# Performance work log

Hardware: AMD Instinct MI355X
Metric: run time of the kernel (lower is better)

## Reference

```python
import jax, jax.numpy as jnp
import numpy as np
import math

B, LQ, LK = 16, 64, 256
EMBED_TIME = 128
H = 8
DK = EMBED_TIME // H  # 16
DIM = 48              # input_dim (num clinical variables)
NHIDDEN = 128


def setup_inputs() -> dict:
    key = jax.random.key(0)
    ks = jax.random.split(key, 10)
    query = jax.random.normal(ks[0], (B, LQ, EMBED_TIME), dtype=jnp.float32)
    key_t = jax.random.normal(ks[1], (B, LK, EMBED_TIME), dtype=jnp.float32)
    value = jax.random.normal(ks[2], (B, LK, DIM), dtype=jnp.float32)
    mask = jax.random.randint(ks[3], (B, LK, DIM), 0, 2, dtype=jnp.int32)
    s = 0.02
    Wq = jax.random.normal(ks[4], (EMBED_TIME, EMBED_TIME), dtype=jnp.float32) * s
    bq = jnp.zeros((EMBED_TIME,), dtype=jnp.float32)
    Wk = jax.random.normal(ks[5], (EMBED_TIME, EMBED_TIME), dtype=jnp.float32) * s
    bk = jnp.zeros((EMBED_TIME,), dtype=jnp.float32)
    Wo = jax.random.normal(ks[6], (NHIDDEN, DIM * H), dtype=jnp.float32) * s
    bo = jnp.zeros((NHIDDEN,), dtype=jnp.float32)
    return {"query": query, "key": key_t, "value": value, "mask": mask,
            "Wq": Wq, "bq": bq, "Wk": Wk, "bk": bk, "Wo": Wo, "bo": bo}


def reference(query, key, value, mask, Wq, bq, Wk, bk, Wo, bo):
    # query: [B, Lq, E], key: [B, Lk, E], value: [B, Lk, D], mask: [B, Lk, D]
    b, lk, d = value.shape
    # time-embedding projections, split into heads: [B, H, L, DK]
    q = (query @ Wq.T + bq).reshape(b, -1, H, DK).transpose(0, 2, 1, 3)
    k = (key @ Wk.T + bk).reshape(b, -1, H, DK).transpose(0, 2, 1, 3)
    # scores: [B, H, Lq, Lk]
    scores = jnp.einsum('bhqd,bhkd->bhqk', q, k) / math.sqrt(DK)
    # expand over value dim (original repeat_interleave) -> [B, H, Lq, Lk, D]
    scores = scores[..., None]
    mask5 = mask[:, None, None, :, :]  # [B,1,1,Lk,D]
    scores = jnp.where(mask5 == 0, jnp.float32(-10000.0), scores)
    # softmax over the key/time axis (-2), per value-dimension
    p_attn = jax.nn.softmax(scores, axis=-2)  # [B,H,Lq,Lk,D]
    # weighted sum over keys: value broadcast over heads & queries
    x = jnp.sum(p_attn * value[:, None, None, :, :], axis=-2)  # [B,H,Lq,D]
    x = x.transpose(0, 2, 1, 3).reshape(b, -1, H * d)  # [B,Lq,H*D]
    return x @ Wo.T + bo  # [B, Lq, nhidden]
```

## Files before the change

### kernel.cpp

```cpp
#include <hip/hip_runtime.h>

#define BB 16
#define LQ 64
#define LK 256
#define EM 128
#define NH 8
#define DKK 16
#define DIM 48
#define NHID 128

#define QP_OFF  0
#define KP_OFF  (BB*LQ*EM)
#define XX_OFF  (KP_OFF + BB*LK*EM)
#define MVM_OFF (XX_OFF + BB*LQ*NH*DIM)

__global__ __launch_bounds__(128) void proj_prep_kernel(
    const float* __restrict__ query, const float* __restrict__ key,
    const float* __restrict__ value, const int* __restrict__ mask,
    const float* __restrict__ Wq, const float* __restrict__ bq,
    const float* __restrict__ Wk, const float* __restrict__ bk,
    float* __restrict__ ws)
{
    int bid = blockIdx.x;
    int t = threadIdx.x;
    if (bid < 640) {
        __shared__ __align__(16) float sX[8][EM];
        int row0 = bid * 8;
        const float* X; const float* W; const float* bias; float* out; int base;
        if (row0 < BB * LQ) { X = query; W = Wq; bias = bq; out = ws + QP_OFF; base = row0; }
        else                { X = key;   W = Wk; bias = bk; out = ws + KP_OFF; base = row0 - BB * LQ; }

        {
            const float4* src = (const float4*)(X + (size_t)base * EM);
            float4* dst = (float4*)(&sX[0][0]);
            #pragma unroll
            for (int u = 0; u < 2; u++) dst[t + u * 128] = src[t + u * 128];
        }
        __syncthreads();

        float acc[8];
        #pragma unroll
        for (int r = 0; r < 8; r++) acc[r] = 0.f;

        const float4* w4 = (const float4*)(W + (size_t)t * EM);
        #pragma unroll 8
        for (int k4 = 0; k4 < EM / 4; k4++) {
            float4 w = w4[k4];
            #pragma unroll
            for (int r = 0; r < 8; r++) {
                float4 x = ((const float4*)sX[r])[k4];
                acc[r] += x.x * w.x + x.y * w.y + x.z * w.z + x.w * w.w;
            }
        }
        float bb = bias[t];
        #pragma unroll
        for (int r = 0; r < 8; r++) out[(size_t)(base + r) * EM + t] = acc[r] + bb;
    } else {
        int p = bid - 640;
        int b = p >> 3, ks = p & 7;
        const float* vb = value + ((size_t)b * LK + ks * 32) * DIM;
        const int*   mb = mask  + ((size_t)b * LK + ks * 32) * DIM;
        float* ob = ws + MVM_OFF + ((size_t)b * LK + ks * 32) * 96;
        #pragma unroll
        for (int u = 0; u < 6; ++u) {
            int f = t + 128 * u;
            int r = f / 24, c = f - r * 24;
            float4 o;
            if (c < 12) {
                float4 v = *(const float4*)(vb + r * DIM + c * 4);
                int4  m  = *(const int4*)  (mb + r * DIM + c * 4);
                o.x = m.x ? v.x : 0.f; o.y = m.y ? v.y : 0.f;
                o.z = m.z ? v.z : 0.f; o.w = m.w ? v.w : 0.f;
            } else {
                int4 m = *(const int4*)(mb + r * DIM + (c - 12) * 4);
                o.x = m.x ? 1.f : 0.f; o.y = m.y ? 1.f : 0.f;
                o.z = m.z ? 1.f : 0.f; o.w = m.w ? 1.f : 0.f;
            }
            *(float4*)(ob + r * 96 + c * 4) = o;
        }
    }
}

__global__ __launch_bounds__(256) void attn_kernel(
    const float* __restrict__ qp, const float* __restrict__ kp,
    const float* __restrict__ mvm, float* __restrict__ xx)
{
    __shared__ __align__(16) float sQ[16][DKK];
    __shared__ __align__(16) float sE[LK][20];
    __shared__ __align__(16) float sW[64][100];

    int bid = blockIdx.x;
    int b  = bid >> 5;
    int h  = (bid >> 2) & 7;
    int q0 = (bid & 3) * 16;
    int t  = threadIdx.x;

    const float4* krp = (const float4*)(kp + ((size_t)b * LK + t) * EM + h * DKK);
    float4 k0 = krp[0], k1 = krp[1], k2 = krp[2], k3 = krp[3];
    if (t < 64) {
        int row = t >> 2, u = t & 3;
        *(float4*)&sQ[row][u * 4] =
            *(const float4*)(qp + ((size_t)b * LQ + q0 + row) * EM + h * DKK + u * 4);
    }
    __syncthreads();

    #pragma unroll
    for (int q4 = 0; q4 < 4; ++q4) {
        float4 ev;
        float* evp = (float*)&ev;
        #pragma unroll
        for (int qi = 0; qi < 4; ++qi) {
            const float4* qr = (const float4*)sQ[q4 * 4 + qi];
            float4 a = qr[0], c = qr[1], d = qr[2], e2 = qr[3];
            float s = k0.x*a.x + k0.y*a.y + k0.z*a.z + k0.w*a.w
                    + k1.x*c.x + k1.y*c.y + k1.z*c.z + k1.w*c.w
                    + k2.x*d.x + k2.y*d.y + k2.z*d.z + k2.w*d.w
                    + k3.x*e2.x + k3.y*e2.y + k3.z*e2.z + k3.w*e2.w;
            evp[qi] = __expf(s * 0.25f);
        }
        *(float4*)&sE[t][q4 * 4] = ev;
    }

    const float* mvb = mvm + (size_t)b * LK * 96;
    auto stage = [&](int kq) {
        const float* src = mvb + (size_t)kq * 64 * 96;
        #pragma unroll
        for (int u = 0; u < 6; ++u) {
            int f = t + 256 * u;
            int r = f / 24, c = f - r * 24;
            *(float4*)&sW[r][c * 4] = *(const float4*)(src + r * 96 + c * 4);
        }
    };
    stage(0);
    __syncthreads();

    int q  = t & 15;
    int kl = (t >> 4) & 3;
    int w  = t >> 6;

    float4 acc[6];
    #pragma unroll
    for (int c = 0; c < 6; ++c) acc[c] = make_float4(0.f, 0.f, 0.f, 0.f);

    for (int kq = 0; kq < 4; ++kq) {
        #pragma unroll 4
        for (int i = 0; i < 16; ++i) {
            int k = kl + 4 * i;
            float ev = sE[kq * 64 + k][q];
            const float4* row = (const float4*)&sW[k][0];
            #pragma unroll
            for (int c = 0; c < 6; ++c) {
                float4 m = row[w * 6 + c];
                acc[c].x += ev * m.x; acc[c].y += ev * m.y;
                acc[c].z += ev * m.z; acc[c].w += ev * m.w;
            }
        }
        __syncthreads();
        if (kq < 3) { stage(kq + 1); __syncthreads(); }
    }

    #pragma unroll
    for (int c = 0; c < 6; ++c) {
        acc[c].x += __shfl_xor(acc[c].x, 16, 64);
        acc[c].y += __shfl_xor(acc[c].y, 16, 64);
        acc[c].z += __shfl_xor(acc[c].z, 16, 64);
        acc[c].w += __shfl_xor(acc[c].w, 16, 64);
        acc[c].x += __shfl_xor(acc[c].x, 32, 64);
        acc[c].y += __shfl_xor(acc[c].y, 32, 64);
        acc[c].z += __shfl_xor(acc[c].z, 32, 64);
        acc[c].w += __shfl_xor(acc[c].w, 32, 64);
    }

    float* zbuf = &sW[0][0];
    if (kl == 0 && w >= 2) {
        #pragma unroll
        for (int c = 0; c < 6; ++c)
            *(float4*)&zbuf[q * 48 + (w - 2) * 24 + c * 4] = acc[c];
    }
    __syncthreads();
    if (kl == 0 && w < 2) {
        float* xr = xx + ((size_t)b * LQ + q0 + q) * (NH * DIM) + h * DIM + w * 24;
        #pragma unroll
        for (int c = 0; c < 6; ++c) {
            float4 z = *(const float4*)&zbuf[q * 48 + w * 24 + c * 4];
            float4 n = acc[c];
            float4 r;
            r.x = n.x / z.x; r.y = n.y / z.y; r.z = n.z / z.z; r.w = n.w / z.w;
            *(float4*)(xr + c * 4) = r;
        }
    }
}

__global__ __launch_bounds__(128) void outproj_kernel(
    const float* __restrict__ x, const float* __restrict__ Wo,
    const float* __restrict__ bo, float* __restrict__ out)
{
    __shared__ __align__(16) float sX[4][NH * DIM];
    int row0 = blockIdx.x * 4;
    int t = threadIdx.x;
    {
        const float4* src = (const float4*)(x + (size_t)row0 * (NH * DIM));
        float4* dst = (float4*)(&sX[0][0]);
        #pragma unroll
        for (int u = 0; u < 3; u++) dst[t + u * 128] = src[t + u * 128];
    }
    __syncthreads();

    float acc[4] = {0.f, 0.f, 0.f, 0.f};
    const float4* w4 = (const float4*)(Wo + (size_t)t * (NH * DIM));
    #pragma unroll 8
    for (int k4 = 0; k4 < (NH * DIM) / 4; k4++) {
        float4 w = w4[k4];
        #pragma unroll
        for (int r = 0; r < 4; r++) {
            float4 xv = ((const float4*)sX[r])[k4];
            acc[r] += xv.x * w.x + xv.y * w.y + xv.z * w.z + xv.w * w.w;
        }
    }
    float bb = bo[t];
    #pragma unroll
    for (int r = 0; r < 4; r++) out[(size_t)(row0 + r) * NHID + t] = acc[r] + bb;
}

extern "C" void kernel_launch(void* const* d_in, const int* in_sizes, int n_in,
                              void* d_out, int out_size, void* d_ws, size_t ws_size,
                              hipStream_t stream) {
    const float* query = (const float*)d_in[0];
    const float* key   = (const float*)d_in[1];
    const float* value = (const float*)d_in[2];
    const int*   mask  = (const int*)  d_in[3];
    const float* Wq    = (const float*)d_in[4];
    const float* bq    = (const float*)d_in[5];
    const float* Wk    = (const float*)d_in[6];
    const float* bk    = (const float*)d_in[7];
    const float* Wo    = (const float*)d_in[8];
    const float* bo    = (const float*)d_in[9];
    float* out = (float*)d_out;
    float* ws = (float*)d_ws;

    proj_prep_kernel<<<dim3(768), dim3(128), 0, stream>>>(
        query, key, value, mask, Wq, bq, Wk, bk, ws);
    attn_kernel<<<dim3(BB * NH * 4), dim3(256), 0, stream>>>(
        ws + QP_OFF, ws + KP_OFF, ws + MVM_OFF, ws + XX_OFF);
    outproj_kernel<<<dim3(BB * LQ / 4), dim3(128), 0, stream>>>(
        ws + XX_OFF, Wo, bo, out);
}
```

Baseline: 53.01 us.

## Fuse mask/value prep into attention kernel and register-tile the accumulation

```diff
diff --git a/kernel.cpp b/kernel.cpp
--- a/kernel.cpp
+++ b/kernel.cpp
@@ -9,84 +9,57 @@
 #define DIM 48
 #define NHID 128
 
-#define QP_OFF  0
-#define KP_OFF  (BB*LQ*EM)
-#define XX_OFF  (KP_OFF + BB*LK*EM)
-#define MVM_OFF (XX_OFF + BB*LQ*NH*DIM)
-
-__global__ __launch_bounds__(128) void proj_prep_kernel(
+#define QP_OFF 0
+#define KP_OFF (BB*LQ*EM)
+#define XX_OFF (KP_OFF + BB*LK*EM)
+
+__global__ __launch_bounds__(128) void proj_kernel(
     const float* __restrict__ query, const float* __restrict__ key,
-    const float* __restrict__ value, const int* __restrict__ mask,
     const float* __restrict__ Wq, const float* __restrict__ bq,
     const float* __restrict__ Wk, const float* __restrict__ bk,
     float* __restrict__ ws)
 {
-    int bid = blockIdx.x;
+    __shared__ __align__(16) float sX[8][EM];
+    int row0 = blockIdx.x * 8;
     int t = threadIdx.x;
-    if (bid < 640) {
-        __shared__ __align__(16) float sX[8][EM];
-        int row0 = bid * 8;
-        const float* X; const float* W; const float* bias; float* out; int base;
-        if (row0 < BB * LQ) { X = query; W = Wq; bias = bq; out = ws + QP_OFF; base = row0; }
-        else                { X = key;   W = Wk; bias = bk; out = ws + KP_OFF; base = row0 - BB * LQ; }
-
-        {
-            const float4* src = (const float4*)(X + (size_t)base * EM);
-            float4* dst = (float4*)(&sX[0][0]);
-            #pragma unroll
-            for (int u = 0; u < 2; u++) dst[t + u * 128] = src[t + u * 128];
-        }
-        __syncthreads();
-
-        float acc[8];
-        #pragma unroll
-        for (int r = 0; r < 8; r++) acc[r] = 0.f;
-
-        const float4* w4 = (const float4*)(W + (size_t)t * EM);
-        #pragma unroll 8
-        for (int k4 = 0; k4 < EM / 4; k4++) {
-            float4 w = w4[k4];
-            #pragma unroll
-            for (int r = 0; r < 8; r++) {
-                float4 x = ((const float4*)sX[r])[k4];
-                acc[r] += x.x * w.x + x.y * w.y + x.z * w.z + x.w * w.w;
-            }
-        }
-        float bb = bias[t];
-        #pragma unroll
-        for (int r = 0; r < 8; r++) out[(size_t)(base + r) * EM + t] = acc[r] + bb;
-    } else {
-        int p = bid - 640;
-        int b = p >> 3, ks = p & 7;
-        const float* vb = value + ((size_t)b * LK + ks * 32) * DIM;
-        const int*   mb = mask  + ((size_t)b * LK + ks * 32) * DIM;
-        float* ob = ws + MVM_OFF + ((size_t)b * LK + ks * 32) * 96;
-        #pragma unroll
-        for (int u = 0; u < 6; ++u) {
-            int f = t + 128 * u;
-            int r = f / 24, c = f - r * 24;
-            float4 o;
-            if (c < 12) {
-                float4 v = *(const float4*)(vb + r * DIM + c * 4);
-                int4  m  = *(const int4*)  (mb + r * DIM + c * 4);
-                o.x = m.x ? v.x : 0.f; o.y = m.y ? v.y : 0.f;
-                o.z = m.z ? v.z : 0.f; o.w = m.w ? v.w : 0.f;
-            } else {
-                int4 m = *(const int4*)(mb + r * DIM + (c - 12) * 4);
-                o.x = m.x ? 1.f : 0.f; o.y = m.y ? 1.f : 0.f;
-                o.z = m.z ? 1.f : 0.f; o.w = m.w ? 1.f : 0.f;
-            }
-            *(float4*)(ob + r * 96 + c * 4) = o;
-        }
-    }
+    const float* X; const float* W; const float* bias; float* out; int base;
+    if (row0 < BB * LQ) { X = query; W = Wq; bias = bq; out = ws + QP_OFF; base = row0; }
+    else                { X = key;   W = Wk; bias = bk; out = ws + KP_OFF; base = row0 - BB * LQ; }
+
+    {
+        const float4* src = (const float4*)(X + (size_t)base * EM);
+        float4* dst = (float4*)(&sX[0][0]);
+        dst[t] = src[t];
+        dst[t + 128] = src[t + 128];
+    }
+    __syncthreads();
+
+    float acc[8];
+    #pragma unroll
+    for (int r = 0; r < 8; r++) acc[r] = 0.f;
+
+    const float4* w4 = (const float4*)(W + (size_t)t * EM);
+    #pragma unroll 8
+    for (int k4 = 0; k4 < EM / 4; k4++) {
+        float4 w = w4[k4];
+        #pragma unroll
+        for (int r = 0; r < 8; r++) {
+            float4 x = ((const float4*)sX[r])[k4];
+            acc[r] += x.x * w.x + x.y * w.y + x.z * w.z + x.w * w.w;
+        }
+    }
+    float bb = bias[t];
+    #pragma unroll
+    for (int r = 0; r < 8; r++) out[(size_t)(base + r) * EM + t] = acc[r] + bb;
 }
 
 __global__ __launch_bounds__(256) void attn_kernel(
     const float* __restrict__ qp, const float* __restrict__ kp,
-    const float* __restrict__ mvm, float* __restrict__ xx)
+    const float* __restrict__ value, const int* __restrict__ mask,
+    float* __restrict__ xx)
 {
     __shared__ __align__(16) float sQ[16][DKK];
-    __shared__ __align__(16) float sE[LK][20];
+    __shared__ __align__(16) float sE[64][20];
     __shared__ __align__(16) float sW[64][100];
 
     int bid = blockIdx.x;
@@ -95,99 +68,135 @@
     int q0 = (bid & 3) * 16;
     int t  = threadIdx.x;
 
-    const float4* krp = (const float4*)(kp + ((size_t)b * LK + t) * EM + h * DKK);
-    float4 k0 = krp[0], k1 = krp[1], k2 = krp[2], k3 = krp[3];
     if (t < 64) {
-        int row = t >> 2, u = t & 3;
-        *(float4*)&sQ[row][u * 4] =
-            *(const float4*)(qp + ((size_t)b * LQ + q0 + row) * EM + h * DKK + u * 4);
-    }
-    __syncthreads();
-
-    #pragma unroll
-    for (int q4 = 0; q4 < 4; ++q4) {
-        float4 ev;
-        float* evp = (float*)&ev;
-        #pragma unroll
-        for (int qi = 0; qi < 4; ++qi) {
-            const float4* qr = (const float4*)sQ[q4 * 4 + qi];
-            float4 a = qr[0], c = qr[1], d = qr[2], e2 = qr[3];
-            float s = k0.x*a.x + k0.y*a.y + k0.z*a.z + k0.w*a.w
-                    + k1.x*c.x + k1.y*c.y + k1.z*c.z + k1.w*c.w
-                    + k2.x*d.x + k2.y*d.y + k2.z*d.z + k2.w*d.w
-                    + k3.x*e2.x + k3.y*e2.y + k3.z*e2.z + k3.w*e2.w;
-            evp[qi] = __expf(s * 0.25f);
-        }
-        *(float4*)&sE[t][q4 * 4] = ev;
-    }
-
-    const float* mvb = mvm + (size_t)b * LK * 96;
-    auto stage = [&](int kq) {
-        const float* src = mvb + (size_t)kq * 64 * 96;
+        int r = t >> 2, u = t & 3;
+        *(float4*)&sQ[r][u * 4] =
+            *(const float4*)(qp + (size_t)(b * LQ + q0 + r) * EM + h * DKK + u * 4);
+    }
+
+    int kr = t & 63;
+    int qg = t >> 6;
+    int kl = t & 7;
+    int qb = (t >> 3) & 3;
+    int jg = t >> 5;
+
+    float acc[4][12];
+    #pragma unroll
+    for (int qi = 0; qi < 4; ++qi)
+        #pragma unroll
+        for (int j = 0; j < 12; ++j) acc[qi][j] = 0.f;
+
+    const float* vb = value + (size_t)b * LK * DIM;
+    const int*   mb = mask  + (size_t)b * LK * DIM;
+
+    __syncthreads();
+
+    for (int c = 0; c < 4; ++c) {
+        int kc = c * 64;
+        {
+            const float4* krow = (const float4*)(kp + (size_t)(b * LK + kc + kr) * EM + h * DKK);
+            float4 k0 = krow[0], k1 = krow[1], k2 = krow[2], k3 = krow[3];
+            float4 ev;
+            float* evp = (float*)&ev;
+            #pragma unroll
+            for (int qi = 0; qi < 4; ++qi) {
+                const float4* qrow = (const float4*)sQ[qg * 4 + qi];
+                float4 a = qrow[0], b2 = qrow[1], c2 = qrow[2], d2 = qrow[3];
+                float s = k0.x*a.x + k0.y*a.y + k0.z*a.z + k0.w*a.w
+                        + k1.x*b2.x + k1.y*b2.y + k1.z*b2.z + k1.w*b2.w
+                        + k2.x*c2.x + k2.y*c2.y + k2.z*c2.z + k2.w*c2.w
+                        + k3.x*d2.x + k3.y*d2.y + k3.z*d2.z + k3.w*d2.w;
+                evp[qi] = __expf(s * 0.25f);
+            }
+            *(float4*)&sE[kr][qg * 4] = ev;
+        }
         #pragma unroll
         for (int u = 0; u < 6; ++u) {
             int f = t + 256 * u;
-            int r = f / 24, c = f - r * 24;
-            *(float4*)&sW[r][c * 4] = *(const float4*)(src + r * 96 + c * 4);
-        }
-    };
-    stage(0);
-    __syncthreads();
-
-    int q  = t & 15;
-    int kl = (t >> 4) & 3;
-    int w  = t >> 6;
-
-    float4 acc[6];
-    #pragma unroll
-    for (int c = 0; c < 6; ++c) acc[c] = make_float4(0.f, 0.f, 0.f, 0.f);
-
-    for (int kq = 0; kq < 4; ++kq) {
-        #pragma unroll 4
-        for (int i = 0; i < 16; ++i) {
-            int k = kl + 4 * i;
-            float ev = sE[kq * 64 + k][q];
-            const float4* row = (const float4*)&sW[k][0];
+            int r = f / 24, cs = f - r * 24;
+            float4 o;
+            if (cs < 12) {
+                float4 v = *(const float4*)(vb + (size_t)(kc + r) * DIM + cs * 4);
+                int4  m  = *(const int4*)  (mb + (size_t)(kc + r) * DIM + cs * 4);
+                o.x = m.x ? v.x : 0.f; o.y = m.y ? v.y : 0.f;
+                o.z = m.z ? v.z : 0.f; o.w = m.w ? v.w : 0.f;
+            } else {
+                int4 m = *(const int4*)(mb + (size_t)(kc + r) * DIM + (cs - 12) * 4);
+                o.x = m.x ? 1.f : 0.f; o.y = m.y ? 1.f : 0.f;
+                o.z = m.z ? 1.f : 0.f; o.w = m.w ? 1.f : 0.f;
+            }
+            *(float4*)&sW[r][cs * 4] = o;
+        }
+        __syncthreads();
+        #pragma unroll
+        for (int i = 0; i < 8; ++i) {
+            int k = kl + 8 * i;
+            float4 e4 = *(const float4*)&sE[k][qb * 4];
+            const float4* wr = (const float4*)&sW[k][jg * 12];
+            float4 w0 = wr[0], w1 = wr[1], w2 = wr[2];
+            float* ep = (float*)&e4;
             #pragma unroll
-            for (int c = 0; c < 6; ++c) {
-                float4 m = row[w * 6 + c];
-                acc[c].x += ev * m.x; acc[c].y += ev * m.y;
-                acc[c].z += ev * m.z; acc[c].w += ev * m.w;
+            for (int qi = 0; qi < 4; ++qi) {
+                float e = ep[qi];
+                acc[qi][0]  += e * w0.x; acc[qi][1]  += e * w0.y;
+                acc[qi][2]  += e * w0.z; acc[qi][3]  += e * w0.w;
+                acc[qi][4]  += e * w1.x; acc[qi][5]  += e * w1.y;
+                acc[qi][6]  += e * w1.z; acc[qi][7]  += e * w1.w;
+                acc[qi][8]  += e * w2.x; acc[qi][9]  += e * w2.y;
+                acc[qi][10] += e * w2.z; acc[qi][11] += e * w2.w;
             }
         }
         __syncthreads();
-        if (kq < 3) { stage(kq + 1); __syncthreads(); }
-    }
-
-    #pragma unroll
-    for (int c = 0; c < 6; ++c) {
-        acc[c].x += __shfl_xor(acc[c].x, 16, 64);
-        acc[c].y += __shfl_xor(acc[c].y, 16, 64);
-        acc[c].z += __shfl_xor(acc[c].z, 16, 64);
-        acc[c].w += __shfl_xor(acc[c].w, 16, 64);
-        acc[c].x += __shfl_xor(acc[c].x, 32, 64);
-        acc[c].y += __shfl_xor(acc[c].y, 32, 64);
-        acc[c].z += __shfl_xor(acc[c].z, 32, 64);
-        acc[c].w += __shfl_xor(acc[c].w, 32, 64);
-    }
-
-    float* zbuf = &sW[0][0];
-    if (kl == 0 && w >= 2) {
-        #pragma unroll
-        for (int c = 0; c < 6; ++c)
-            *(float4*)&zbuf[q * 48 + (w - 2) * 24 + c * 4] = acc[c];
-    }
-    __syncthreads();
-    if (kl == 0 && w < 2) {
-        float* xr = xx + ((size_t)b * LQ + q0 + q) * (NH * DIM) + h * DIM + w * 24;
-        #pragma unroll
-        for (int c = 0; c < 6; ++c) {
-            float4 z = *(const float4*)&zbuf[q * 48 + w * 24 + c * 4];
-            float4 n = acc[c];
-            float4 r;
-            r.x = n.x / z.x; r.y = n.y / z.y; r.z = n.z / z.z; r.w = n.w / z.w;
-            *(float4*)(xr + c * 4) = r;
-        }
+    }
+
+    float v48[48];
+    #pragma unroll
+    for (int qi = 0; qi < 4; ++qi)
+        #pragma unroll
+        for (int j = 0; j < 12; ++j) v48[qi * 12 + j] = acc[qi][j];
+
+    bool hi1 = (kl & 1) != 0;
+    float s1[24];
+    #pragma unroll
+    for (int i = 0; i < 24; ++i) {
+        float keep = hi1 ? v48[24 + i] : v48[i];
+        float send = hi1 ? v48[i] : v48[24 + i];
+        s1[i] = keep + __shfl_xor(send, 1, 64);
+    }
+    bool hi2 = (kl & 2) != 0;
+    float s2[12];
+    #pragma unroll
+    for (int i = 0; i < 12; ++i) {
+        float keep = hi2 ? s1[12 + i] : s1[i];
+        float send = hi2 ? s1[i] : s1[12 + i];
+        s2[i] = keep + __shfl_xor(send, 2, 64);
+    }
+    bool hi3 = (kl & 4) != 0;
+    float s3[6];
+    #pragma unroll
+    for (int i = 0; i < 6; ++i) {
+        float keep = hi3 ? s2[6 + i] : s2[i];
+        float send = hi3 ? s2[i] : s2[6 + i];
+        s3[i] = keep + __shfl_xor(send, 4, 64);
+    }
+
+    int base = (hi1 ? 24 : 0) + (hi2 ? 12 : 0) + (hi3 ? 6 : 0);
+    int qi = base / 12;
+    int j0 = base - qi * 12;
+    int q  = qb * 4 + qi;
+
+    float* sZ = &sE[0][0];
+    if (jg >= 4) {
+        int jz = (jg - 4) * 12 + j0;
+        #pragma unroll
+        for (int i = 0; i < 6; ++i) sZ[q * 52 + jz + i] = s3[i];
+    }
+    __syncthreads();
+    if (jg < 4) {
+        int j = jg * 12 + j0;
+        float* xr = xx + (size_t)(b * LQ + q0 + q) * (NH * DIM) + h * DIM + j;
+        #pragma unroll
+        for (int i = 0; i < 6; ++i) xr[i] = s3[i] / sZ[q * 52 + j + i];
     }
 }
 
@@ -238,10 +247,10 @@
     float* out = (float*)d_out;
     float* ws = (float*)d_ws;
 
-    proj_prep_kernel<<<dim3(768), dim3(128), 0, stream>>>(
-        query, key, value, mask, Wq, bq, Wk, bk, ws);
+    proj_kernel<<<dim3((BB*LQ + BB*LK) / 8), dim3(128), 0, stream>>>(
+        query, key, Wq, bq, Wk, bk, ws);
     attn_kernel<<<dim3(BB * NH * 4), dim3(256), 0, stream>>>(
-        ws + QP_OFF, ws + KP_OFF, ws + MVM_OFF, ws + XX_OFF);
+        ws + QP_OFF, ws + KP_OFF, value, mask, ws + XX_OFF);
     outproj_kernel<<<dim3(BB * LQ / 4), dim3(128), 0, stream>>>(
         ws + XX_OFF, Wo, bo, out);
 }
```

Result: slower. 57.56 us (+8.6%).
